# Kernel tuning notes

Measured on AMD Instinct MI355X. Metric: run time of the kernel, lower is better.

Reference implementation:

```python
import jax, jax.numpy as jnp
import numpy as np

RADIUS = 0.15
DECAY_RADIUS = 0.3
BN_EPS = 1e-5


def batchnorm(x, gamma, beta):
    # x: [B, N, C]; training-mode BN over (B, N) per channel (matches nn.BatchNorm1d on [B,C,N])
    mu = x.mean(axis=(0, 1))
    var = x.var(axis=(0, 1))
    return gamma * (x - mu) * jax.lax.rsqrt(var + BN_EPS) + beta


def aggregate(mutual, xyz, radius, decay_radius):
    # mutual: [B, N, 6*C]; xyz: [B, N, 3]
    # For each point i, weighted sum over neighbors j within decay_radius.
    # Direction weights: squared cosine with the 6 axis-aligned bases (+x,-x,+y,-y,+z,-z).
    # Distance weight: 1 inside radius, linear decay to 0 at decay_radius. Output normalized by weight sum.
    B, N, C6 = mutual.shape
    C = C6 // 6
    r2, dr2 = radius * radius, decay_radius * decay_radius
    # per-axis pairwise differences diff_a[b,i,j] = xyz[b,j,a] - xyz[b,i,a]
    dxs = [xyz[:, None, :, a] - xyz[:, :, None, a] for a in range(3)]
    d2 = dxs[0] ** 2 + dxs[1] ** 2 + dxs[2] ** 2
    valid = (d2 < dr2) & (d2 > 0.0)
    wd = jnp.where(d2 <= r2, 1.0, (dr2 - d2) / (dr2 - r2))
    wd = jnp.where(valid, wd, 0.0)  # [B,N,N]
    inv_d2 = wd / jnp.maximum(d2, 1e-12)  # fuse distance weight with 1/d2 for cos^2
    groups = mutual.reshape(B, N, 6, C)
    out = jnp.zeros((B, N, C), mutual.dtype)
    for a in range(3):
        comp = dxs[a]
        wpos = inv_d2 * jnp.square(jnp.maximum(comp, 0.0))
        wneg = inv_d2 * jnp.square(jnp.maximum(-comp, 0.0))
        out = out + jnp.einsum('bij,bjc->bic', wpos, groups[:, :, 2 * a, :])
        out = out + jnp.einsum('bij,bjc->bic', wneg, groups[:, :, 2 * a + 1, :])
    norm = wd.sum(axis=-1)  # [B,N]
    out = out / jnp.maximum(norm, 1e-12)[..., None]
    return out, norm


def setup_inputs() -> dict:
    key = jax.random.key(0)
    ks = jax.random.split(key, 12)
    B, N, Cin, Cout, Cb = 16, 2048, 64, 64, 32
    feat = jax.random.normal(ks[0], (B, N, Cin), jnp.float32)
    xyz = jax.random.uniform(ks[1], (B, N, 3), jnp.float32)
    s = 1.0 / np.sqrt(Cin)
    W_feat = jax.random.uniform(ks[2], (Cin, Cout), jnp.float32, -s, s)
    b_feat = jax.random.uniform(ks[3], (Cout,), jnp.float32, -s, s)
    W_byp = jax.random.uniform(ks[4], (Cin, 6 * Cb), jnp.float32, -s, s)  # bias=False (bn on)
    g_byp = jnp.ones((6 * Cb,), jnp.float32)
    be_byp = jnp.zeros((6 * Cb,), jnp.float32)
    g1 = jnp.ones((Cb,), jnp.float32)
    be1 = jnp.zeros((Cb,), jnp.float32)
    sb = 1.0 / np.sqrt(Cb)
    W_ag = jax.random.uniform(ks[5], (Cb, Cout), jnp.float32, -sb, sb)
    b_ag = jax.random.uniform(ks[6], (Cout,), jnp.float32, -sb, sb)
    g2 = jnp.ones((Cout,), jnp.float32)
    be2 = jnp.zeros((Cout,), jnp.float32)
    return {"feat": feat, "xyz": xyz, "W_feat": W_feat, "b_feat": b_feat,
            "W_byp": W_byp, "g_byp": g_byp, "be_byp": be_byp,
            "g1": g1, "be1": be1, "W_ag": W_ag, "b_ag": b_ag, "g2": g2, "be2": be2}


def reference(feat, xyz, W_feat, b_feat, W_byp, g_byp, be_byp, g1, be1, W_ag, b_ag, g2, be2):
    self_feat = feat @ W_feat + b_feat                        # [B,N,Cout]
    mutual = jax.nn.relu(batchnorm(feat @ W_byp, g_byp, be_byp))  # Fc: linear->BN->relu, [B,N,6*Cb]
    ag, _ = aggregate(mutual, xyz, RADIUS, DECAY_RADIUS)      # [B,N,Cb]
    ag = jax.nn.relu(batchnorm(ag, g1, be1))
    ag = ag @ W_ag + b_ag                                     # [B,N,Cout]
    out = jax.nn.relu(batchnorm(self_feat + ag, g2, be2))
    return out
```

## Files before the change

### kernel.cpp

```cpp
#include <hip/hip_runtime.h>
#include <cstddef>

#define NPTS   2048
#define NB     16
#define MROWS  (NPTS*NB)
#define BN_EPS 1e-5f

typedef __attribute__((ext_vector_type(8))) short bf16x8;
typedef __attribute__((ext_vector_type(4))) float f32x4;
typedef __attribute__((ext_vector_type(2))) float f32x2;

__device__ inline unsigned cvtpk(float a, float b) {
    unsigned r;
    asm("v_cvt_pk_bf16_f32 %0, %1, %2" : "=v"(r) : "v"(a), "v"(b));
    return r;
}
__device__ inline unsigned cvtpk_abs(float a, float b) {
    unsigned r;
    asm("v_cvt_pk_bf16_f32 %0, |%1|, |%2|" : "=v"(r) : "v"(a), "v"(b));
    return r;
}

union U4 { unsigned u[4]; bf16x8 v; };

__global__ __launch_bounds__(256) void prep_k(
    const float* __restrict__ Wf, const float* __restrict__ Wb,
    const float* __restrict__ Wag, const float* __restrict__ xyz,
    unsigned short* __restrict__ Wpk, unsigned short* __restrict__ Wpk2,
    float* __restrict__ xT)
{
    const int bid = blockIdx.x;
    if (bid < 8) {
        const int gid  = bid*256 + threadIdx.x;
        const int lane = gid & 63;
        const int n    = ((gid >> 7) << 4) + (lane & 15);
        const int k0   = (((gid >> 6) & 1) << 5) + ((lane >> 4) << 3);
        unsigned o[4];
        #pragma unroll
        for (int p = 0; p < 4; ++p) {
            const int ka = k0 + 2*p, kb = ka + 1;
            const float va = (n < 64) ? Wf[ka*64 + n] : Wb[ka*192 + (n - 64)];
            const float vb = (n < 64) ? Wf[kb*64 + n] : Wb[kb*192 + (n - 64)];
            o[p] = cvtpk(va, vb);
        }
        uint4 ov = { o[0], o[1], o[2], o[3] };
        *(uint4*)(Wpk + (size_t)gid * 8) = ov;
    } else if (bid == 8) {
        const int g2   = threadIdx.x;
        const int lane = g2 & 63;
        const int nt   = g2 >> 6;
        const int n    = nt*16 + (lane & 15);
        const int k0   = (lane >> 4) * 8;
        unsigned o[4];
        #pragma unroll
        for (int p = 0; p < 4; ++p) {
            const int ka = k0 + 2*p, kb = ka + 1;
            o[p] = cvtpk(Wag[ka*64 + n], Wag[kb*64 + n]);
        }
        uint4 ov = { o[0], o[1], o[2], o[3] };
        *(uint4*)(Wpk2 + (size_t)g2 * 8) = ov;
    } else {
        const int t = (bid - 9) * 256 + threadIdx.x;
        if (t < NB*NPTS) {
            const int b = t >> 11, j = t & (NPTS-1);
            const float* p = xyz + (size_t)t * 3;
            xT[((size_t)b*3 + 0)*NPTS + j] = p[0];
            xT[((size_t)b*3 + 1)*NPTS + j] = p[1];
            xT[((size_t)b*3 + 2)*NPTS + j] = p[2];
        }
    }
}

__global__ __launch_bounds__(256) void linear1_mfma_k(
    const float* __restrict__ feat, const unsigned short* __restrict__ Wpk,
    const float* __restrict__ bf,
    float* __restrict__ selfF, float* __restrict__ preB,
    float* __restrict__ s192s, float* __restrict__ s192q)
{
    __shared__ float lps[4][12][16];
    __shared__ float lpq[4][12][16];
    const int t    = threadIdx.x;
    const int lane = t & 63;
    const int w    = t >> 6;
    const int r0   = blockIdx.x * 64 + w * 16;
    const int mrow = lane & 15;
    const int kgrp = lane >> 4;

    U4 Afr[2];
    #pragma unroll
    for (int ks = 0; ks < 2; ++ks) {
        const float* src = feat + (size_t)(r0 + mrow)*64 + ks*32 + kgrp*8;
        const float4 v0 = *(const float4*)src;
        const float4 v1 = *(const float4*)(src + 4);
        Afr[ks].u[0] = cvtpk(v0.x, v0.y);
        Afr[ks].u[1] = cvtpk(v0.z, v0.w);
        Afr[ks].u[2] = cvtpk(v1.x, v1.y);
        Afr[ks].u[3] = cvtpk(v1.z, v1.w);
    }

    #pragma unroll 4
    for (int nt = 0; nt < 16; ++nt) {
        const unsigned short* wp = Wpk + (size_t)(nt*2)*512 + lane*8;
        const bf16x8 B0 = *(const bf16x8*)(wp);
        const bf16x8 B1 = *(const bf16x8*)(wp + 512);
        f32x4 acc = {0.f, 0.f, 0.f, 0.f};
        acc = __builtin_amdgcn_mfma_f32_16x16x32_bf16(Afr[0].v, B0, acc, 0,0,0);
        acc = __builtin_amdgcn_mfma_f32_16x16x32_bf16(Afr[1].v, B1, acc, 0,0,0);

        const int ncol = nt*16 + mrow;
        if (nt < 4) {
            const float bias = bf[ncol];
            #pragma unroll
            for (int r = 0; r < 4; ++r)
                selfF[(size_t)(r0 + kgrp*4 + r)*64 + ncol] = acc[r] + bias;
        } else {
            float s = 0.f, q = 0.f;
            #pragma unroll
            for (int r = 0; r < 4; ++r) {
                const float v = acc[r];
                preB[(size_t)(r0 + kgrp*4 + r)*192 + (ncol - 64)] = v;
                s += v; q = fmaf(v, v, q);
            }
            s += __shfl_xor(s, 16);  s += __shfl_xor(s, 32);
            q += __shfl_xor(q, 16);  q += __shfl_xor(q, 32);
            if (lane < 16) {
                lps[w][nt-4][lane] = s;
                lpq[w][nt-4][lane] = q;
            }
        }
    }
    __syncthreads();
    if (t < 192) {
        const int ni = t >> 4, la = t & 15;
        const float s = lps[0][ni][la] + lps[1][ni][la] + lps[2][ni][la] + lps[3][ni][la];
        const float q = lpq[0][ni][la] + lpq[1][ni][la] + lpq[2][ni][la] + lpq[3][ni][la];
        atomicAdd(s192s + t, s);
        atomicAdd(s192q + t, q);
    }
}

__global__ __launch_bounds__(256) void bn_t192_k(
    const float* __restrict__ sum, const float* __restrict__ sq,
    const float* __restrict__ g,   const float* __restrict__ be,
    const float* __restrict__ X,   unsigned short* __restrict__ mTf)
{
    __shared__ float ltile[64][65];
    const int bid = blockIdx.x;
    const int ax  = bid % 3;
    const int jb  = (bid / 3) % 32;
    const int b   = bid / 96;
    const int t   = threadIdx.x;

    const int cl = t & 63;
    const int c  = ax*64 + cl;
    const float invM = 1.0f / (float)MROWS;
    const float mu  = sum[c] * invM;
    const float var = sq[c] * invM - mu*mu;
    const float sc  = g[c] * rsqrtf(var + BN_EPS);
    const float sh  = be[c] - mu * sc;

    const float* __restrict__ Xb = X + ((size_t)b*NPTS + jb*64) * 192;
    #pragma unroll
    for (int rr = 0; rr < 16; ++rr) {
        const int j = (t >> 6) + rr*4;
        const float v = Xb[(size_t)j*192 + c];
        ltile[cl][j] = fmaxf(fmaf(v, sc, sh), 0.0f);
    }
    __syncthreads();

    const int lane = t & 63;
    const int h    = (t >> 6) & 1;
    const int sd   = (t >> 7) & 1;
    const int cc   = h*16 + (lane & 15);
    const int jB   = (lane >> 4) * 8;
    const float sgn = sd ? 0.5f : -0.5f;
    #pragma unroll
    for (int js = 0; js < 2; ++js) {
        unsigned o[4];
        #pragma unroll
        for (int p = 0; p < 4; ++p) {
            const int j = js*32 + jB + 2*p;
            const float vlo = fmaf(ltile[cc+32][j],   sgn, ltile[cc][j]   * 0.5f);
            const float vhi = fmaf(ltile[cc+32][j+1], sgn, ltile[cc][j+1] * 0.5f);
            o[p] = cvtpk(vlo, vhi);
        }
        const int slot = ax*2 + sd;
        unsigned short* dst = mTf + ((((size_t)(b*64 + jb*2 + js)*6 + slot)*2 + h)*64 + lane)*8;
        uint4 ov = { o[0], o[1], o[2], o[3] };
        *(uint4*)dst = ov;
    }
}

__global__ __launch_bounds__(256) void aggregate_mfma_k(
    const unsigned short* __restrict__ mTf,
    const float* __restrict__ xT,
    float* __restrict__ agp,
    float* __restrict__ nrmp)
{
    __shared__ float lacc[4][32][32];
    __shared__ float lnorm[4][32];

    const int bid = blockIdx.x;
    const int swz = (bid & 7) * 256 + (bid >> 3);
    const int b     = swz >> 7;
    const int rem   = swz & 127;
    const int i0    = (rem >> 1) << 5;
    const int jhalf = rem & 1;
    const int t    = threadIdx.x;
    const int lane = t & 63;
    const int w    = t >> 6;
    const int iloc = lane & 15;
    const int kgrp = lane >> 4;

    const float* __restrict__ xb = xT + (size_t)b * 3 * NPTS;
    const unsigned short* __restrict__ mb = mTf + (size_t)b * 64 * 12 * 512;

    const float xi0 = xb[0*NPTS + i0 + iloc],      yi0 = xb[1*NPTS + i0 + iloc],      zi0 = xb[2*NPTS + i0 + iloc];
    const float xi1 = xb[0*NPTS + i0 + 16 + iloc], yi1 = xb[1*NPTS + i0 + 16 + iloc], zi1 = xb[2*NPTS + i0 + 16 + iloc];

    f32x4 acc[2][2];
    #pragma unroll
    for (int a = 0; a < 2; ++a)
        #pragma unroll
        for (int h = 0; h < 2; ++h) acc[a][h] = f32x4{0.f,0.f,0.f,0.f};
    float nrm0 = 0.0f, nrm1 = 0.0f;

    const float dr2   = 0.30f*0.30f;
    const float invdr = 1.0f / (dr2 - 0.15f*0.15f);
    const float drc   = dr2 * invdr;
    const f32x2 mind2 = {-invdr, -invdr};
    const f32x2 drc2  = {drc, drc};

    const int jbase = jhalf*1024 + w*256;
    for (int j0 = jbase; j0 < jbase + 256; j0 += 32) {
        const int jj = j0 + kgrp*8;
        const float4 a0 = *(const float4*)(xb + 0*NPTS + jj);
        const float4 a1 = *(const float4*)(xb + 0*NPTS + jj + 4);
        const float4 b0 = *(const float4*)(xb + 1*NPTS + jj);
        const float4 b1 = *(const float4*)(xb + 1*NPTS + jj + 4);
        const float4 c0 = *(const float4*)(xb + 2*NPTS + jj);
        const float4 c1 = *(const float4*)(xb + 2*NPTS + jj + 4);
        const f32x2 px[4] = {{a0.x,a0.y},{a0.z,a0.w},{a1.x,a1.y},{a1.z,a1.w}};
        const f32x2 py[4] = {{b0.x,b0.y},{b0.z,b0.w},{b1.x,b1.y},{b1.z,b1.w}};
        const f32x2 pz[4] = {{c0.x,c0.y},{c0.z,c0.w},{c1.x,c1.y},{c1.z,c1.w}};

        U4 pwS[2][3], pwA[2][3];
        #pragma unroll
        for (int it = 0; it < 2; ++it) {
            const float xi = it ? xi1 : xi0;
            const float yi = it ? yi1 : yi0;
            const float zi = it ? zi1 : zi0;
            const f32x2 xi2 = {xi, xi};
            const f32x2 yi2 = {yi, yi};
            const f32x2 zi2 = {zi, zi};
            #pragma unroll
            for (int p = 0; p < 4; ++p) {
                const f32x2 dx = px[p] - xi2;
                const f32x2 dy = py[p] - yi2;
                const f32x2 dz = pz[p] - zi2;
                const f32x2 d2 = dx*dx + dy*dy + dz*dz;
                const f32x2 wdl = d2*mind2 + drc2;
                const float wd0 = __builtin_amdgcn_fmed3f(wdl.x, 0.0f, 1.0f);
                const float wd1 = __builtin_amdgcn_fmed3f(wdl.y, 0.0f, 1.0f);
                if (it) { nrm1 += wd0; nrm1 += wd1; }
                else    { nrm0 += wd0; nrm0 += wd1; }
                const f32x2 inv2 = { wd0 * __builtin_amdgcn_rcpf(fmaxf(d2.x, 1e-12f)),
                                     wd1 * __builtin_amdgcn_rcpf(fmaxf(d2.y, 1e-12f)) };
                #pragma unroll
                for (int ax = 0; ax < 3; ++ax) {
                    const f32x2 da = (ax == 0) ? dx : (ax == 1) ? dy : dz;
                    const f32x2 u = da * inv2;
                    const float s0 = u.x * __builtin_fabsf(da.x);
                    const float s1 = u.y * __builtin_fabsf(da.y);
                    pwS[it][ax].u[p] = cvtpk(s0, s1);
                    pwA[it][ax].u[p] = cvtpk_abs(s0, s1);
                }
            }
        }

        const unsigned short* sb = mb + (size_t)(j0 >> 5) * 12 * 512 + lane*8;
        #pragma unroll
        for (int ax = 0; ax < 3; ++ax) {
            #pragma unroll
            for (int h = 0; h < 2; ++h) {
                const bf16x8 Bd = *(const bf16x8*)(sb + (size_t)((2*ax  )*2 + h)*512);
                const bf16x8 Bs = *(const bf16x8*)(sb + (size_t)((2*ax+1)*2 + h)*512);
                acc[0][h] = __builtin_amdgcn_mfma_f32_16x16x32_bf16(pwS[0][ax].v, Bd, acc[0][h], 0,0,0);
                acc[0][h] = __builtin_amdgcn_mfma_f32_16x16x32_bf16(pwA[0][ax].v, Bs, acc[0][h], 0,0,0);
                acc[1][h] = __builtin_amdgcn_mfma_f32_16x16x32_bf16(pwS[1][ax].v, Bd, acc[1][h], 0,0,0);
                acc[1][h] = __builtin_amdgcn_mfma_f32_16x16x32_bf16(pwA[1][ax].v, Bs, acc[1][h], 0,0,0);
            }
        }
    }

    nrm0 += __shfl_xor(nrm0, 16);  nrm0 += __shfl_xor(nrm0, 32);
    nrm1 += __shfl_xor(nrm1, 16);  nrm1 += __shfl_xor(nrm1, 32);

    #pragma unroll
    for (int it = 0; it < 2; ++it)
        #pragma unroll
        for (int r = 0; r < 4; ++r) {
            lacc[w][it*16 + kgrp*4 + r][iloc]      = acc[it][0][r];
            lacc[w][it*16 + kgrp*4 + r][16 + iloc] = acc[it][1][r];
        }
    if (lane < 16) { lnorm[w][lane] = nrm0; lnorm[w][16 + lane] = nrm1; }
    __syncthreads();

    float* agh = agp + (size_t)jhalf * MROWS * 32;
    #pragma unroll
    for (int rep = 0; rep < 4; ++rep) {
        const int idx = t + rep*256;
        const int i = idx >> 5, c = idx & 31;
        const float s = lacc[0][i][c] + lacc[1][i][c] + lacc[2][i][c] + lacc[3][i][c];
        agh[((size_t)b*NPTS + i0 + i)*32 + c] = s;
    }
    if (t < 32) {
        const float n = lnorm[0][t] + lnorm[1][t] + lnorm[2][t] + lnorm[3][t];
        nrmp[(size_t)jhalf*MROWS + b*NPTS + i0 + t] = n;
    }
}

__global__ __launch_bounds__(256) void finalize_k(
    const float* __restrict__ agp, const float* __restrict__ nrmp,
    float* __restrict__ ag, float* __restrict__ s32s, float* __restrict__ s32q)
{
    __shared__ float lv[64][33];
    const int t  = threadIdx.x;
    const int r0 = blockIdx.x * 64;

    #pragma unroll
    for (int rep = 0; rep < 2; ++rep) {
        const int lidx = t + rep*256;
        const int rl = lidx >> 3;
        const int c0 = (lidx & 7) * 4;
        const size_t r = (size_t)r0 + rl;
        const float4 p0 = *(const float4*)(agp + r*32 + c0);
        const float4 p1 = *(const float4*)(agp + ((size_t)MROWS + r)*32 + c0);
        const float n = nrmp[r] + nrmp[MROWS + r] - 1.0f;
        const float invn = __builtin_amdgcn_rcpf(fmaxf(n, 1e-12f));
        float4 v;
        v.x = (p0.x + p1.x) * invn;  v.y = (p0.y + p1.y) * invn;
        v.z = (p0.z + p1.z) * invn;  v.w = (p0.w + p1.w) * invn;
        *(float4*)(ag + r*32 + c0) = v;
        lv[rl][c0] = v.x; lv[rl][c0+1] = v.y; lv[rl][c0+2] = v.z; lv[rl][c0+3] = v.w;
    }
    __syncthreads();
    if (t < 32) {
        float ps = 0.0f, pq = 0.0f;
        #pragma unroll
        for (int i = 0; i < 64; ++i) {
            const float v = lv[i][t];
            ps += v; pq = fmaf(v, v, pq);
        }
        atomicAdd(s32s + t, ps);
        atomicAdd(s32q + t, pq);
    }
}

__global__ __launch_bounds__(256) void lin2f_mfma_k(
    const float* __restrict__ ag,
    const float* __restrict__ s32s, const float* __restrict__ s32q,
    const float* __restrict__ g1,   const float* __restrict__ be1,
    const unsigned short* __restrict__ Wpk2,
    const float* __restrict__ bag,  const float* __restrict__ selfF,
    float* __restrict__ pre2,
    float* __restrict__ s64s, float* __restrict__ s64q)
{
    __shared__ float sc_[32], sh_[32];
    __shared__ float lps[4][4][16];
    __shared__ float lpq[4][4][16];
    const int t    = threadIdx.x;
    const int lane = t & 63;
    const int w    = t >> 6;
    const int r0   = blockIdx.x * 64 + w * 16;
    const int mrow = lane & 15;
    const int kgrp = lane >> 4;

    if (t < 32) {
        const float invM = 1.0f / (float)MROWS;
        const float mu  = s32s[t] * invM;
        const float var = s32q[t] * invM - mu*mu;
        const float sc  = g1[t] * rsqrtf(var + BN_EPS);
        sc_[t] = sc; sh_[t] = be1[t] - mu * sc;
    }
    __syncthreads();

    U4 Afr;
    {
        const float* src = ag + (size_t)(r0 + mrow)*32 + kgrp*8;
        const float4 v0 = *(const float4*)src;
        const float4 v1 = *(const float4*)(src + 4);
        const int c0 = kgrp*8;
        const float vv[8] = {v0.x,v0.y,v0.z,v0.w,v1.x,v1.y,v1.z,v1.w};
        float bn[8];
        #pragma unroll
        for (int e = 0; e < 8; ++e)
            bn[e] = fmaxf(fmaf(vv[e], sc_[c0+e], sh_[c0+e]), 0.0f);
        Afr.u[0] = cvtpk(bn[0], bn[1]);
        Afr.u[1] = cvtpk(bn[2], bn[3]);
        Afr.u[2] = cvtpk(bn[4], bn[5]);
        Afr.u[3] = cvtpk(bn[6], bn[7]);
    }

    #pragma unroll
    for (int nt = 0; nt < 4; ++nt) {
        const bf16x8 B = *(const bf16x8*)(Wpk2 + (size_t)nt*512 + lane*8);
        f32x4 acc = {0.f,0.f,0.f,0.f};
        acc = __builtin_amdgcn_mfma_f32_16x16x32_bf16(Afr.v, B, acc, 0,0,0);

        const int ncol = nt*16 + mrow;
        const float bias = bag[ncol];
        float s = 0.f, q = 0.f;
        #pragma unroll
        for (int r = 0; r < 4; ++r) {
            const int row = r0 + kgrp*4 + r;
            const float val = acc[r] + bias + selfF[(size_t)row*64 + ncol];
            pre2[(size_t)row*64 + ncol] = val;
            s += val; q = fmaf(val, val, q);
        }
        s += __shfl_xor(s, 16);  s += __shfl_xor(s, 32);
        q += __shfl_xor(q, 16);  q += __shfl_xor(q, 32);
        if (lane < 16) { lps[w][nt][lane] = s; lpq[w][nt][lane] = q; }
    }
    __syncthreads();
    if (t < 64) {
        const int nt = t >> 4, la = t & 15;
        const float s = lps[0][nt][la] + lps[1][nt][la] + lps[2][nt][la] + lps[3][nt][la];
        const float q = lpq[0][nt][la] + lpq[1][nt][la] + lpq[2][nt][la] + lpq[3][nt][la];
        atomicAdd(s64s + t, s);
        atomicAdd(s64q + t, q);
    }
}

template<int C>
__global__ __launch_bounds__(256) void bn_relu_k(
    const float* __restrict__ sum, const float* __restrict__ sq,
    const float* __restrict__ g,   const float* __restrict__ be,
    const float* __restrict__ X, float* __restrict__ Y, int n4)
{
    __shared__ __align__(16) float ssc[C];
    __shared__ __align__(16) float ssh[C];
    const int t = threadIdx.x;
    if (t < C) {
        const float invM = 1.0f / (float)MROWS;
        const float mu  = sum[t] * invM;
        const float var = sq[t] * invM - mu*mu;
        const float sc  = g[t] * rsqrtf(var + BN_EPS);
        ssc[t] = sc;
        ssh[t] = be[t] - mu * sc;
    }
    __syncthreads();
    const float4* __restrict__ X4 = (const float4*)X;
    float4* __restrict__ Y4 = (float4*)Y;
    const int stride = gridDim.x * 256;
    for (int i = blockIdx.x*256 + t; i < n4; i += stride) {
        const int c4 = i % (C/4);
        float4 v = X4[i];
        const float4 sc = ((const float4*)ssc)[c4];
        const float4 sh = ((const float4*)ssh)[c4];
        v.x = fmaxf(fmaf(v.x, sc.x, sh.x), 0.0f);
        v.y = fmaxf(fmaf(v.y, sc.y, sh.y), 0.0f);
        v.z = fmaxf(fmaf(v.z, sc.z, sh.z), 0.0f);
        v.w = fmaxf(fmaf(v.w, sc.w, sh.w), 0.0f);
        Y4[i] = v;
    }
}

extern "C" void kernel_launch(void* const* d_in, const int* in_sizes, int n_in,
                              void* d_out, int out_size, void* d_ws, size_t ws_size,
                              hipStream_t stream)
{
    const float* feat = (const float*)d_in[0];
    const float* xyz  = (const float*)d_in[1];
    const float* Wf   = (const float*)d_in[2];
    const float* bf   = (const float*)d_in[3];
    const float* Wb   = (const float*)d_in[4];
    const float* gby  = (const float*)d_in[5];
    const float* beby = (const float*)d_in[6];
    const float* g1   = (const float*)d_in[7];
    const float* be1  = (const float*)d_in[8];
    const float* Wag  = (const float*)d_in[9];
    const float* bag  = (const float*)d_in[10];
    const float* g2   = (const float*)d_in[11];
    const float* be2  = (const float*)d_in[12];

    float* ws = (float*)d_ws;
    float* stats = ws;
    float* A   = ws + 1024;
    float* B   = A + (size_t)MROWS*64;
    float* C   = B + (size_t)MROWS*192;
    float* xT  = C + (size_t)MROWS*32;
    unsigned short* mTf  = (unsigned short*)(xT + (size_t)NB*3*NPTS);
    unsigned short* Wpk  = mTf + (size_t)NB*64*12*512;
    unsigned short* Wpk2 = Wpk + 16384;
    float* agp  = B;
    float* nrmp = B + (size_t)MROWS*64;
    float* D = B;

    float* s192s = stats;       float* s192q = stats + 192;
    float* s32s  = stats + 384; float* s32q  = stats + 416;
    float* s64s  = stats + 448; float* s64q  = stats + 512;

    (void)hipMemsetAsync(stats, 0, 1024 * sizeof(float), stream);

    prep_k<<<137, 256, 0, stream>>>(Wf, Wb, Wag, xyz, Wpk, Wpk2, xT);
    linear1_mfma_k<<<512, 256, 0, stream>>>(feat, Wpk, bf, A, B, s192s, s192q);

    bn_t192_k<<<1536, 256, 0, stream>>>(s192s, s192q, gby, beby, B, mTf);

    aggregate_mfma_k<<<2048, 256, 0, stream>>>(mTf, xT, agp, nrmp);

    finalize_k<<<512, 256, 0, stream>>>(agp, nrmp, C, s32s, s32q);

    lin2f_mfma_k<<<512, 256, 0, stream>>>(C, s32s, s32q, g1, be1, Wpk2, bag, A, D, s64s, s64q);

    bn_relu_k<64><<<512, 256, 0, stream>>>(s64s, s64q, g2, be2, D, (float*)d_out, MROWS*64/4);
}
```

Before: 131.6 us.

## Fuse finalize, linear2 and final BN-ReLU into one cooperative kernel

Replaces three tail kernels with one cooperative kernel that keeps the aggregated features and the pre-BN output tile in shared memory, using grid-wide syncs to wait for the batch-norm statistics. This removes two launches and the global round trips for the intermediate ag and pre2 buffers. In exchange it needs all 512 blocks to be co-resident, uses extra LDS (about 25KB per block), and pays the cost of two grid barriers.

```diff
diff --git a/kernel.cpp b/kernel.cpp
--- a/kernel.cpp
+++ b/kernel.cpp
@@ -1,5 +1,8 @@
 #include <hip/hip_runtime.h>
+#include <hip/hip_cooperative_groups.h>
 #include <cstddef>
+
+namespace cg = cooperative_groups;
 
 #define NPTS   2048
 #define NB     16
@@ -320,13 +323,28 @@
     }
 }
 
-__global__ __launch_bounds__(256) void finalize_k(
+__global__ __launch_bounds__(256) void tail_k(
     const float* __restrict__ agp, const float* __restrict__ nrmp,
-    float* __restrict__ ag, float* __restrict__ s32s, float* __restrict__ s32q)
+    float* __restrict__ s32s, float* __restrict__ s32q,
+    const float* __restrict__ g1,  const float* __restrict__ be1,
+    const unsigned short* __restrict__ Wpk2,
+    const float* __restrict__ bag, const float* __restrict__ selfF,
+    float* __restrict__ s64s, float* __restrict__ s64q,
+    const float* __restrict__ g2,  const float* __restrict__ be2,
+    float* __restrict__ out)
 {
+    cg::grid_group grid = cg::this_grid();
     __shared__ float lv[64][33];
+    __shared__ float pre2l[64][65];
+    __shared__ float sc_[64], sh_[64];
+    __shared__ float lps[4][4][16], lpq[4][4][16];
+
     const int t  = threadIdx.x;
     const int r0 = blockIdx.x * 64;
+    const int lane = t & 63;
+    const int w    = t >> 6;
+    const int mrow = lane & 15;
+    const int kgrp = lane >> 4;
 
     #pragma unroll
     for (int rep = 0; rep < 2; ++rep) {
@@ -338,11 +356,10 @@
         const float4 p1 = *(const float4*)(agp + ((size_t)MROWS + r)*32 + c0);
         const float n = nrmp[r] + nrmp[MROWS + r] - 1.0f;
         const float invn = __builtin_amdgcn_rcpf(fmaxf(n, 1e-12f));
-        float4 v;
-        v.x = (p0.x + p1.x) * invn;  v.y = (p0.y + p1.y) * invn;
-        v.z = (p0.z + p1.z) * invn;  v.w = (p0.w + p1.w) * invn;
-        *(float4*)(ag + r*32 + c0) = v;
-        lv[rl][c0] = v.x; lv[rl][c0+1] = v.y; lv[rl][c0+2] = v.z; lv[rl][c0+3] = v.w;
+        lv[rl][c0]   = (p0.x + p1.x) * invn;
+        lv[rl][c0+1] = (p0.y + p1.y) * invn;
+        lv[rl][c0+2] = (p0.z + p1.z) * invn;
+        lv[rl][c0+3] = (p0.w + p1.w) * invn;
     }
     __syncthreads();
     if (t < 32) {
@@ -355,26 +372,7 @@
         atomicAdd(s32s + t, ps);
         atomicAdd(s32q + t, pq);
     }
-}
-
-__global__ __launch_bounds__(256) void lin2f_mfma_k(
-    const float* __restrict__ ag,
-    const float* __restrict__ s32s, const float* __restrict__ s32q,
-    const float* __restrict__ g1,   const float* __restrict__ be1,
-    const unsigned short* __restrict__ Wpk2,
-    const float* __restrict__ bag,  const float* __restrict__ selfF,
-    float* __restrict__ pre2,
-    float* __restrict__ s64s, float* __restrict__ s64q)
-{
-    __shared__ float sc_[32], sh_[32];
-    __shared__ float lps[4][4][16];
-    __shared__ float lpq[4][4][16];
-    const int t    = threadIdx.x;
-    const int lane = t & 63;
-    const int w    = t >> 6;
-    const int r0   = blockIdx.x * 64 + w * 16;
-    const int mrow = lane & 15;
-    const int kgrp = lane >> 4;
+    grid.sync();
 
     if (t < 32) {
         const float invM = 1.0f / (float)MROWS;
@@ -387,15 +385,12 @@
 
     U4 Afr;
     {
-        const float* src = ag + (size_t)(r0 + mrow)*32 + kgrp*8;
-        const float4 v0 = *(const float4*)src;
-        const float4 v1 = *(const float4*)(src + 4);
+        const int rl = w*16 + mrow;
         const int c0 = kgrp*8;
-        const float vv[8] = {v0.x,v0.y,v0.z,v0.w,v1.x,v1.y,v1.z,v1.w};
         float bn[8];
         #pragma unroll
         for (int e = 0; e < 8; ++e)
-            bn[e] = fmaxf(fmaf(vv[e], sc_[c0+e], sh_[c0+e]), 0.0f);
+            bn[e] = fmaxf(fmaf(lv[rl][c0+e], sc_[c0+e], sh_[c0+e]), 0.0f);
         Afr.u[0] = cvtpk(bn[0], bn[1]);
         Afr.u[1] = cvtpk(bn[2], bn[3]);
         Afr.u[2] = cvtpk(bn[4], bn[5]);
@@ -413,9 +408,9 @@
         float s = 0.f, q = 0.f;
         #pragma unroll
         for (int r = 0; r < 4; ++r) {
-            const int row = r0 + kgrp*4 + r;
-            const float val = acc[r] + bias + selfF[(size_t)row*64 + ncol];
-            pre2[(size_t)row*64 + ncol] = val;
+            const int rl = w*16 + kgrp*4 + r;
+            const float val = acc[r] + bias + selfF[(size_t)(r0 + rl)*64 + ncol];
+            pre2l[rl][ncol] = val;
             s += val; q = fmaf(val, val, q);
         }
         s += __shfl_xor(s, 16);  s += __shfl_xor(s, 32);
@@ -430,39 +425,27 @@
         atomicAdd(s64s + t, s);
         atomicAdd(s64q + t, q);
     }
-}
-
-template<int C>
-__global__ __launch_bounds__(256) void bn_relu_k(
-    const float* __restrict__ sum, const float* __restrict__ sq,
-    const float* __restrict__ g,   const float* __restrict__ be,
-    const float* __restrict__ X, float* __restrict__ Y, int n4)
-{
-    __shared__ __align__(16) float ssc[C];
-    __shared__ __align__(16) float ssh[C];
-    const int t = threadIdx.x;
-    if (t < C) {
+    grid.sync();
+
+    if (t < 64) {
         const float invM = 1.0f / (float)MROWS;
-        const float mu  = sum[t] * invM;
-        const float var = sq[t] * invM - mu*mu;
-        const float sc  = g[t] * rsqrtf(var + BN_EPS);
-        ssc[t] = sc;
-        ssh[t] = be[t] - mu * sc;
-    }
-    __syncthreads();
-    const float4* __restrict__ X4 = (const float4*)X;
-    float4* __restrict__ Y4 = (float4*)Y;
-    const int stride = gridDim.x * 256;
-    for (int i = blockIdx.x*256 + t; i < n4; i += stride) {
-        const int c4 = i % (C/4);
-        float4 v = X4[i];
-        const float4 sc = ((const float4*)ssc)[c4];
-        const float4 sh = ((const float4*)ssh)[c4];
-        v.x = fmaxf(fmaf(v.x, sc.x, sh.x), 0.0f);
-        v.y = fmaxf(fmaf(v.y, sc.y, sh.y), 0.0f);
-        v.z = fmaxf(fmaf(v.z, sc.z, sh.z), 0.0f);
-        v.w = fmaxf(fmaf(v.w, sc.w, sh.w), 0.0f);
-        Y4[i] = v;
+        const float mu  = s64s[t] * invM;
+        const float var = s64q[t] * invM - mu*mu;
+        const float sc  = g2[t] * rsqrtf(var + BN_EPS);
+        sc_[t] = sc; sh_[t] = be2[t] - mu * sc;
+    }
+    __syncthreads();
+    #pragma unroll
+    for (int rep = 0; rep < 4; ++rep) {
+        const int lidx = t + rep*256;
+        const int row = lidx >> 4;
+        const int c0  = (lidx & 15) * 4;
+        float4 v;
+        v.x = fmaxf(fmaf(pre2l[row][c0+0], sc_[c0+0], sh_[c0+0]), 0.0f);
+        v.y = fmaxf(fmaf(pre2l[row][c0+1], sc_[c0+1], sh_[c0+1]), 0.0f);
+        v.z = fmaxf(fmaf(pre2l[row][c0+2], sc_[c0+2], sh_[c0+2]), 0.0f);
+        v.w = fmaxf(fmaf(pre2l[row][c0+3], sc_[c0+3], sh_[c0+3]), 0.0f);
+        *(float4*)(out + (size_t)(r0 + row)*64 + c0) = v;
     }
 }
 
@@ -495,7 +478,6 @@
     unsigned short* Wpk2 = Wpk + 16384;
     float* agp  = B;
     float* nrmp = B + (size_t)MROWS*64;
-    float* D = B;
 
     float* s192s = stats;       float* s192q = stats + 192;
     float* s32s  = stats + 384; float* s32q  = stats + 416;
@@ -510,9 +492,16 @@
 
     aggregate_mfma_k<<<2048, 256, 0, stream>>>(mTf, xT, agp, nrmp);
 
-    finalize_k<<<512, 256, 0, stream>>>(agp, nrmp, C, s32s, s32q);
-
-    lin2f_mfma_k<<<512, 256, 0, stream>>>(C, s32s, s32q, g1, be1, Wpk2, bag, A, D, s64s, s64q);
-
-    bn_relu_k<64><<<512, 256, 0, stream>>>(s64s, s64q, g2, be2, D, (float*)d_out, MROWS*64/4);
-}
+    float* outp = (float*)d_out;
+    void* args[] = {
+        (void*)&agp, (void*)&nrmp,
+        (void*)&s32s, (void*)&s32q,
+        (void*)&g1, (void*)&be1,
+        (void*)&Wpk2, (void*)&bag, (void*)&A,
+        (void*)&s64s, (void*)&s64q,
+        (void*)&g2, (void*)&be2,
+        (void*)&outp
+    };
+    (void)hipLaunchCooperativeKernel((void*)tail_k, dim3(512), dim3(256),
+                                     args, 0, stream);
+}
```

Result: slower. 206.2 us (+56.7%).
